# Kernel optimization log

Hardware: AMD Instinct MI355X
Metric: run time of the kernel (lower is better)

## Reference

```python
import jax, jax.numpy as jnp
import numpy as np

# Module hyperparameters (init_kwargs)
TOP_K = 0.15          # fraction of pixels kept per row when step_percent=1
IGNORE_INDEX = 255

B, K, N, H, W = 8, 3, 8, 384, 384


def setup_inputs() -> dict:
    key = jax.random.key(0)
    k1, k2 = jax.random.split(key)
    # log-probabilities over K classes (nll_loss expects log-probs)
    logits = jax.random.normal(k1, (B, K, N, H, W), dtype=jnp.float32)
    inp = jax.nn.log_softmax(logits, axis=1)
    target = jax.random.randint(k2, (B, N, H, W), 0, K, dtype=jnp.int32)
    return {"input": inp, "target": target, "step_percent": 1}


def reference(input, target, step_percent):
    b, k, n, h, w = input.shape
    P = h * w
    x = input.reshape(b * n, k, P)           # (BN, K, P)
    t = target.reshape(b * n, P)             # (BN, P)

    # per-pixel NLL with ignore_index (ignored pixels contribute 0)
    mask = t != IGNORE_INDEX
    t_safe = jnp.where(mask, t, 0)
    nll = -jnp.take_along_axis(x, t_safe[:, None, :], axis=1)[:, 0, :]  # (BN, P)
    nll = jnp.where(mask, nll, jnp.zeros((), nll.dtype))

    # static k: step_percent is a Python scalar in the original forward
    sp = min(float(step_percent), 1.0)
    n_top_k = int(sp * TOP_K * P + (1.0 - sp) * P)

    top_k_loss, _ = jax.lax.top_k(nll, n_top_k)  # (BN, n_top_k)
    return jnp.mean(top_k_loss)
```

## Files before the change

### kernel.cpp

```cpp
#include <hip/hip_runtime.h>

#define BN    64
#define KCLS  3
#define PPIX  147456
#define NB1   4096
#define NB3   128
#define CAP   8192

#define BPR    32
#define F4PB   (PPIX / 4 / BPR)

#define BPR_C  36
#define F4_BLK 1024
#define PX_BLK 4096

#define SCOPE __HIP_MEMORY_SCOPE_AGENT

static const size_t OFF_NLL  = 0;
static const size_t OFF_CAND = OFF_NLL + (size_t)BN * PPIX * 4;
static const size_t OFF_GH   = OFF_CAND + (size_t)BN * CAP * 4;
static const size_t OFF_CCNT = OFF_GH + (size_t)BN * NB1 * 4;
static const size_t OFF_SS   = OFF_CCNT + 256;
static const size_t OFF_ACC  = OFF_SS + 512;
static const size_t OFF_DONE = OFF_ACC + 8;
static const size_t ZERO_END = OFF_DONE + 8;
static const size_t OFF_B1   = ZERO_END;
static const size_t OFF_R1   = ZERO_END + 256;

__device__ __forceinline__ unsigned topk_count(const int* sp_ptr) {
    double sp = (double)sp_ptr[0];
    if (sp > 1.0) sp = 1.0;
    return (unsigned)(sp * 0.15 * (double)PPIX + (1.0 - sp) * (double)PPIX);
}

__device__ __forceinline__ float sel_nll(int t, float a, float b, float c) {
    float lp = (t == 0) ? a : ((t == 1) ? b : ((t == 2) ? c : 0.0f));
    return fmaxf(-lp, 0.0f);
}

__global__ __launch_bounds__(256) void k_hist1(
    const float* __restrict__ in, const int* __restrict__ tgt,
    float* __restrict__ nll, unsigned* __restrict__ cnt1)
{
    __shared__ unsigned lc[NB1];
    const int tid = threadIdx.x;
    for (int i = tid; i < NB1; i += 256) lc[i] = 0u;
    __syncthreads();

    const int row   = blockIdx.x / BPR;
    const int chunk = blockIdx.x % BPR;
    const float4* p0 = (const float4*)(in + (size_t)row * KCLS * PPIX);
    const float4* p1 = p0 + PPIX / 4;
    const float4* p2 = p1 + PPIX / 4;
    const int4*   t4 = (const int4*)(tgt + (size_t)row * PPIX);
    float4*       n4 = (float4*)(nll + (size_t)row * PPIX);
    const int base = chunk * F4PB;
    const bool tail = (tid < (F4PB - 4 * 256));

    int idx_c = base + tid;
    int4   t_c = t4[idx_c];
    float4 a_c = p0[idx_c];
    float4 b_c = p1[idx_c];
    float4 c_c = p2[idx_c];

    #pragma unroll
    for (int j = 0; j < 4; ++j) {
        int idx_n = 0;
        int4 t_n; float4 a_n, b_n, c_n;
        const bool have_next = (j < 3) || tail;
        if (have_next) {
            idx_n = base + (j + 1) * 256 + tid;
            t_n = t4[idx_n];
            a_n = p0[idx_n];
            b_n = p1[idx_n];
            c_n = p2[idx_n];
        }

        float4 v;
        v.x = sel_nll(t_c.x, a_c.x, b_c.x, c_c.x);
        v.y = sel_nll(t_c.y, a_c.y, b_c.y, c_c.y);
        v.z = sel_nll(t_c.z, a_c.z, b_c.z, c_c.z);
        v.w = sel_nll(t_c.w, a_c.w, b_c.w, c_c.w);
        n4[idx_c] = v;
        atomicAdd(&lc[__float_as_uint(v.x) >> 19], 1u);
        atomicAdd(&lc[__float_as_uint(v.y) >> 19], 1u);
        atomicAdd(&lc[__float_as_uint(v.z) >> 19], 1u);
        atomicAdd(&lc[__float_as_uint(v.w) >> 19], 1u);

        idx_c = idx_n; t_c = t_n; a_c = a_n; b_c = b_n; c_c = c_n;
    }

    if (tail) {
        float4 v;
        v.x = sel_nll(t_c.x, a_c.x, b_c.x, c_c.x);
        v.y = sel_nll(t_c.y, a_c.y, b_c.y, c_c.y);
        v.z = sel_nll(t_c.z, a_c.z, b_c.z, c_c.z);
        v.w = sel_nll(t_c.w, a_c.w, b_c.w, c_c.w);
        n4[idx_c] = v;
        atomicAdd(&lc[__float_as_uint(v.x) >> 19], 1u);
        atomicAdd(&lc[__float_as_uint(v.y) >> 19], 1u);
        atomicAdd(&lc[__float_as_uint(v.z) >> 19], 1u);
        atomicAdd(&lc[__float_as_uint(v.w) >> 19], 1u);
    }
    __syncthreads();

    unsigned* gc = cnt1 + (size_t)row * NB1;
    for (int i = tid; i < NB1; i += 256) {
        const unsigned cc = lc[i];
        if (cc) atomicAdd(&gc[i], cc);
    }
}

__global__ __launch_bounds__(256) void k_scan(
    const unsigned* __restrict__ cnt, const int* __restrict__ sp_ptr,
    int* __restrict__ st_b, int* __restrict__ st_r)
{
    const int row = blockIdx.x, tid = threadIdx.x;
    __shared__ unsigned csum[256];
    const unsigned* c = cnt + (size_t)row * NB1;

    unsigned cl[16]; unsigned cacc = 0;
    const int base = tid * 16;
    #pragma unroll
    for (int i = 0; i < 16; ++i) {
        cl[i] = c[NB1 - 1 - (base + i)];
        cacc += cl[i];
    }
    csum[tid] = cacc;
    __syncthreads();
    for (int off = 1; off < 256; off <<= 1) {
        unsigned t2 = (tid >= off) ? csum[tid - off] : 0u;
        __syncthreads();
        csum[tid] += t2;
        __syncthreads();
    }
    const unsigned k = topk_count(sp_ptr);
    unsigned cum = tid ? csum[tid - 1] : 0u;
    #pragma unroll
    for (int i = 0; i < 16; ++i) {
        const unsigned cb = cl[i];
        if (cum < k && cum + cb >= k) {
            st_b[row] = NB1 - 1 - (base + i);
            st_r[row] = (int)(k - cum);
        }
        cum += cb;
    }
}

__global__ __launch_bounds__(256) void k_compact(
    const float* __restrict__ nll, const int* __restrict__ st_b1,
    float* __restrict__ cand, int* __restrict__ ccnt, double* __restrict__ st_S)
{
    __shared__ float  stage[PX_BLK];
    __shared__ double dred[256];
    __shared__ int lcnt, gbase;
    const int tid = threadIdx.x;
    if (tid == 0) lcnt = 0;
    __syncthreads();

    const int row   = blockIdx.x / BPR_C;
    const int chunk = blockIdx.x % BPR_C;
    const unsigned b1 = (unsigned)st_b1[row];
    const unsigned lo = b1 << 19;
    const unsigned hi = (b1 + 1u) << 19;
    const float4* n4 = (const float4*)(nll + (size_t)row * PPIX);
    const int base = chunk * F4_BLK;

    double acc = 0.0;
    #pragma unroll
    for (int j = 0; j < 4; ++j) {
        const float4 f = n4[base + j * 256 + tid];
        const float vv[4] = {f.x, f.y, f.z, f.w};
        #pragma unroll
        for (int q = 0; q < 4; ++q) {
            const unsigned u = __float_as_uint(vv[q]);
            if (u >= hi) {
                acc += (double)vv[q];
            } else if (u >= lo) {
                const int s = atomicAdd(&lcnt, 1);
                stage[s] = vv[q];
            }
        }
    }
    dred[tid] = acc;
    __syncthreads();
    for (int s = 128; s > 0; s >>= 1) {
        if (tid < s) dred[tid] += dred[tid + s];
        __syncthreads();
    }
    if (tid == 0) {
        atomicAdd(&st_S[row], dred[0]);
        gbase = atomicAdd(&ccnt[row], lcnt);
    }
    __syncthreads();
    const int n = lcnt, gb = gbase;
    float* cr = cand + (size_t)row * CAP;
    for (int i = tid; i < n; i += 256) {
        const int pos = gb + i;
        if (pos < CAP) cr[pos] = stage[i];
    }
}

__global__ __launch_bounds__(256) void k_resolve(
    const float* __restrict__ cand, const int* __restrict__ ccnt,
    const int* __restrict__ st_b1, const int* __restrict__ st_r1,
    const double* __restrict__ st_S, const int* __restrict__ sp,
    double* __restrict__ accum, unsigned* __restrict__ done,
    float* __restrict__ out)
{
    __shared__ unsigned lc[NB1];
    __shared__ float    ls[NB1];
    __shared__ unsigned csum[256];
    __shared__ double   ssum[256];
    __shared__ int sb2, sr2;
    __shared__ double sS2;

    const int row = blockIdx.x, tid = threadIdx.x;
    int n = ccnt[row]; if (n > CAP) n = CAP;
    const float* cv = cand + (size_t)row * CAP;

    for (int i = tid; i < NB1; i += 256) { lc[i] = 0u; ls[i] = 0.0f; }
    __syncthreads();
    for (int i = tid; i < n; i += 256) {
        const float v = cv[i];
        const unsigned key = (__float_as_uint(v) >> 7) & 0xFFFu;
        atomicAdd(&lc[key], 1u);
        atomicAdd(&ls[key], v);
    }
    __syncthreads();

    unsigned cl[16]; float slv[16];
    unsigned cacc = 0; double sacc = 0.0;
    const int base = tid * 16;
    #pragma unroll
    for (int i = 0; i < 16; ++i) {
        const int bin = NB1 - 1 - (base + i);
        cl[i]  = lc[bin];
        slv[i] = ls[bin];
        cacc += cl[i];
        sacc += (double)slv[i];
    }
    csum[tid] = cacc; ssum[tid] = sacc;
    __syncthreads();
    for (int off = 1; off < 256; off <<= 1) {
        unsigned cv2 = 0; double sv = 0.0;
        if (tid >= off) { cv2 = csum[tid - off]; sv = ssum[tid - off]; }
        __syncthreads();
        csum[tid] += cv2; ssum[tid] += sv;
        __syncthreads();
    }
    const unsigned k = (unsigned)st_r1[row];
    unsigned cum = tid ? csum[tid - 1] : 0u;
    double   sS  = tid ? ssum[tid - 1] : 0.0;
    #pragma unroll
    for (int i = 0; i < 16; ++i) {
        const unsigned cb = cl[i];
        if (cum < k && cum + cb >= k) {
            sb2 = NB1 - 1 - (base + i);
            sr2 = (int)(k - cum);
            sS2 = sS;
        }
        cum += cb;
        sS  += (double)slv[i];
    }
    __syncthreads();

    const unsigned pref = ((unsigned)st_b1[row] << 12) | (unsigned)sb2;
    if (tid < NB3) { lc[tid] = 0u; ls[tid] = 0.0f; }
    __syncthreads();
    for (int i = tid; i < n; i += 256) {
        const float v = cv[i];
        const unsigned bits = __float_as_uint(v);
        if ((bits >> 7) == pref) {
            atomicAdd(&lc[bits & 0x7Fu], 1u);
            atomicAdd(&ls[bits & 0x7Fu], v);
        }
    }
    __syncthreads();
    if (tid == 0) {
        const unsigned k3 = (unsigned)sr2;
        unsigned cum3 = 0, r3 = 0; int b3 = 0; double S3 = 0.0;
        for (int bin = NB3 - 1; bin >= 0; --bin) {
            const unsigned cb = lc[bin];
            if (cum3 < k3 && cum3 + cb >= k3) { b3 = bin; r3 = k3 - cum3; break; }
            cum3 += cb;
            S3   += (double)ls[bin];
        }
        const float tval = __uint_as_float((pref << 7) | (unsigned)b3);
        const double total = st_S[row] + sS2 + S3 + (double)r3 * (double)tval;
        atomicAdd(accum, total);
        __threadfence();
        const unsigned ticket =
            __hip_atomic_fetch_add(done, 1u, __ATOMIC_ACQ_REL, SCOPE);
        if (ticket == BN - 1) {
            const double a2 =
                __hip_atomic_load(accum, __ATOMIC_RELAXED, SCOPE);
            out[0] = (float)(a2 / ((double)BN * (double)topk_count(sp)));
        }
    }
}

extern "C" void kernel_launch(void* const* d_in, const int* in_sizes, int n_in,
                              void* d_out, int out_size, void* d_ws, size_t ws_size,
                              hipStream_t stream)
{
    (void)in_sizes; (void)n_in; (void)out_size; (void)ws_size;
    const float* in  = (const float*)d_in[0];
    const int*   tgt = (const int*)d_in[1];
    const int*   sp  = (const int*)d_in[2];

    char* ws = (char*)d_ws;
    float*    nll   = (float*)(ws + OFF_NLL);
    float*    cand  = (float*)(ws + OFF_CAND);
    unsigned* ghist = (unsigned*)(ws + OFF_GH);
    int*      ccnt  = (int*)(ws + OFF_CCNT);
    double*   st_S  = (double*)(ws + OFF_SS);
    double*   accum = (double*)(ws + OFF_ACC);
    unsigned* done  = (unsigned*)(ws + OFF_DONE);
    int*      st_b1 = (int*)(ws + OFF_B1);
    int*      st_r1 = (int*)(ws + OFF_R1);

    hipMemsetAsync(ws + OFF_GH, 0, ZERO_END - OFF_GH, stream);

    k_hist1  <<<BN * BPR,   256, 0, stream>>>(in, tgt, nll, ghist);
    k_scan   <<<BN,         256, 0, stream>>>(ghist, sp, st_b1, st_r1);
    k_compact<<<BN * BPR_C, 256, 0, stream>>>(nll, st_b1, cand, ccnt, st_S);
    k_resolve<<<BN,         256, 0, stream>>>(cand, ccnt, st_b1, st_r1, st_S,
                                              sp, accum, done, (float*)d_out);
}
```

Measured before the change: 249.2 us.

## Fuse per-row histogram scan into compaction kernel, drop separate scan launch

```diff
diff --git a/kernel.cpp b/kernel.cpp
--- a/kernel.cpp
+++ b/kernel.cpp
@@ -9,10 +9,7 @@
 
 #define BPR    32
 #define F4PB   (PPIX / 4 / BPR)
-
-#define BPR_C  36
-#define F4_BLK 1024
-#define PX_BLK 4096
+#define PXB    (F4PB * 4)
 
 #define SCOPE __HIP_MEMORY_SCOPE_AGENT
 
@@ -111,64 +108,67 @@
     }
 }
 
-__global__ __launch_bounds__(256) void k_scan(
-    const unsigned* __restrict__ cnt, const int* __restrict__ sp_ptr,
+__global__ __launch_bounds__(256) void k_scompact(
+    const float* __restrict__ nll, const unsigned* __restrict__ ghist,
+    const int* __restrict__ sp, float* __restrict__ cand,
+    int* __restrict__ ccnt, double* __restrict__ st_S,
     int* __restrict__ st_b, int* __restrict__ st_r)
 {
-    const int row = blockIdx.x, tid = threadIdx.x;
-    __shared__ unsigned csum[256];
-    const unsigned* c = cnt + (size_t)row * NB1;
-
-    unsigned cl[16]; unsigned cacc = 0;
-    const int base = tid * 16;
-    #pragma unroll
-    for (int i = 0; i < 16; ++i) {
-        cl[i] = c[NB1 - 1 - (base + i)];
-        cacc += cl[i];
-    }
-    csum[tid] = cacc;
-    __syncthreads();
-    for (int off = 1; off < 256; off <<= 1) {
-        unsigned t2 = (tid >= off) ? csum[tid - off] : 0u;
+    __shared__ float  stage[PXB];
+    __shared__ double wsum[4];
+    __shared__ int s_b1, s_r1, lcnt, gbase;
+
+    const int tid   = threadIdx.x;
+    const int row   = blockIdx.x / BPR;
+    const int chunk = blockIdx.x % BPR;
+
+    {
+        unsigned* csum = (unsigned*)stage;
+        const unsigned* c = ghist + (size_t)row * NB1;
+        unsigned cl[16]; unsigned cacc = 0;
+        const int base = tid * 16;
+        #pragma unroll
+        for (int i = 0; i < 16; ++i) {
+            cl[i] = c[NB1 - 1 - (base + i)];
+            cacc += cl[i];
+        }
+        csum[tid] = cacc;
         __syncthreads();
-        csum[tid] += t2;
-        __syncthreads();
-    }
-    const unsigned k = topk_count(sp_ptr);
-    unsigned cum = tid ? csum[tid - 1] : 0u;
-    #pragma unroll
-    for (int i = 0; i < 16; ++i) {
-        const unsigned cb = cl[i];
-        if (cum < k && cum + cb >= k) {
-            st_b[row] = NB1 - 1 - (base + i);
-            st_r[row] = (int)(k - cum);
-        }
-        cum += cb;
-    }
-}
-
-__global__ __launch_bounds__(256) void k_compact(
-    const float* __restrict__ nll, const int* __restrict__ st_b1,
-    float* __restrict__ cand, int* __restrict__ ccnt, double* __restrict__ st_S)
-{
-    __shared__ float  stage[PX_BLK];
-    __shared__ double dred[256];
-    __shared__ int lcnt, gbase;
-    const int tid = threadIdx.x;
-    if (tid == 0) lcnt = 0;
-    __syncthreads();
-
-    const int row   = blockIdx.x / BPR_C;
-    const int chunk = blockIdx.x % BPR_C;
-    const unsigned b1 = (unsigned)st_b1[row];
+        for (int off = 1; off < 256; off <<= 1) {
+            unsigned t2 = (tid >= off) ? csum[tid - off] : 0u;
+            __syncthreads();
+            csum[tid] += t2;
+            __syncthreads();
+        }
+        const unsigned k = topk_count(sp);
+        unsigned cum = tid ? csum[tid - 1] : 0u;
+        #pragma unroll
+        for (int i = 0; i < 16; ++i) {
+            const unsigned cb = cl[i];
+            if (cum < k && cum + cb >= k) {
+                s_b1 = NB1 - 1 - (base + i);
+                s_r1 = (int)(k - cum);
+            }
+            cum += cb;
+        }
+        if (tid == 0) lcnt = 0;
+    }
+    __syncthreads();
+    if (chunk == 0 && tid == 0) {
+        st_b[row] = s_b1;
+        st_r[row] = s_r1;
+    }
+
+    const unsigned b1 = (unsigned)s_b1;
     const unsigned lo = b1 << 19;
     const unsigned hi = (b1 + 1u) << 19;
     const float4* n4 = (const float4*)(nll + (size_t)row * PPIX);
-    const int base = chunk * F4_BLK;
+    const int base = chunk * F4PB;
 
     double acc = 0.0;
     #pragma unroll
-    for (int j = 0; j < 4; ++j) {
+    for (int j = 0; j < 5; ++j) {
+        if (j == 4 && tid >= (F4PB - 4 * 256)) break;
         const float4 f = n4[base + j * 256 + tid];
         const float vv[4] = {f.x, f.y, f.z, f.w};
         #pragma unroll
@@ -182,17 +182,17 @@
             }
         }
     }
-    dred[tid] = acc;
-    __syncthreads();
-    for (int s = 128; s > 0; s >>= 1) {
-        if (tid < s) dred[tid] += dred[tid + s];
-        __syncthreads();
-    }
+
+    #pragma unroll
+    for (int off = 32; off > 0; off >>= 1) acc += __shfl_down(acc, off, 64);
+    if ((tid & 63) == 0) wsum[tid >> 6] = acc;
+    __syncthreads();
     if (tid == 0) {
-        atomicAdd(&st_S[row], dred[0]);
+        atomicAdd(&st_S[row], (wsum[0] + wsum[1]) + (wsum[2] + wsum[3]));
         gbase = atomicAdd(&ccnt[row], lcnt);
     }
     __syncthreads();
+
     const int n = lcnt, gb = gbase;
     float* cr = cand + (size_t)row * CAP;
     for (int i = tid; i < n; i += 256) {
@@ -322,9 +322,9 @@
 
     hipMemsetAsync(ws + OFF_GH, 0, ZERO_END - OFF_GH, stream);
 
-    k_hist1  <<<BN * BPR,   256, 0, stream>>>(in, tgt, nll, ghist);
-    k_scan   <<<BN,         256, 0, stream>>>(ghist, sp, st_b1, st_r1);
-    k_compact<<<BN * BPR_C, 256, 0, stream>>>(nll, st_b1, cand, ccnt, st_S);
-    k_resolve<<<BN,         256, 0, stream>>>(cand, ccnt, st_b1, st_r1, st_S,
-                                              sp, accum, done, (float*)d_out);
-}
+    k_hist1   <<<BN * BPR, 256, 0, stream>>>(in, tgt, nll, ghist);
+    k_scompact<<<BN * BPR, 256, 0, stream>>>(nll, ghist, sp, cand, ccnt, st_S,
+                                             st_b1, st_r1);
+    k_resolve <<<BN,       256, 0, stream>>>(cand, ccnt, st_b1, st_r1, st_S,
+                                             sp, accum, done, (float*)d_out);
+}
```

Result: no change. 246.4 us (-1.2%).
